# Performance work log

Measured on AMD Instinct MI355X. Metric: run time of the kernel, lower is better.

The kernel has to match this reference:

```python
import jax, jax.numpy as jnp
import numpy as np

D_MODEL = 128
NHEAD = 8
HEAD_DIM = D_MODEL // NHEAD  # 16
NUM_LAYERS = 7
NUM_LABELS = 2
N_NODES = 10000
N_EDGES = 160000
NEG_SLOPE = 0.2  # GATv2Conv default negative_slope


def setup_inputs() -> dict:
    key = jax.random.key(0)
    ks = jax.random.split(key, 10)
    s = 1.0 / np.sqrt(D_MODEL)
    inp = {}
    inp["x"] = jax.random.normal(ks[0], (N_NODES, D_MODEL), dtype=jnp.float32)
    inp["edge_index"] = jax.random.randint(ks[1], (2, N_EDGES), 0, N_NODES, dtype=jnp.int64)
    inp["nchunks"] = 8  # uniform extra chunk size -> chunk = NUM_LABELS + 8 = 10
    # per-layer GATv2 params, stacked on a leading layer axis
    inp["Wl"] = jax.random.normal(ks[2], (NUM_LAYERS, D_MODEL, NHEAD * HEAD_DIM), dtype=jnp.float32) * s
    inp["bl"] = jnp.zeros((NUM_LAYERS, NHEAD * HEAD_DIM), dtype=jnp.float32)
    inp["Wr"] = jax.random.normal(ks[3], (NUM_LAYERS, D_MODEL, NHEAD * HEAD_DIM), dtype=jnp.float32) * s
    inp["br"] = jnp.zeros((NUM_LAYERS, NHEAD * HEAD_DIM), dtype=jnp.float32)
    inp["att"] = jax.random.normal(ks[4], (NUM_LAYERS, NHEAD, HEAD_DIM), dtype=jnp.float32) * s
    inp["bias"] = jnp.zeros((NUM_LAYERS, NHEAD * HEAD_DIM), dtype=jnp.float32)
    # split head: Linear(d_model, 1)
    inp["w_head"] = jax.random.normal(ks[5], (D_MODEL, 1), dtype=jnp.float32) * s
    inp["b_head"] = jnp.zeros((1,), dtype=jnp.float32)
    return inp


def _gatv2_layer(x, src, dst, Wl, bl, Wr, br, att, bias):
    # GATv2: e_ij = a^T LeakyReLU(W_l x_j + W_r x_i); alpha = segment-softmax over dst; out_i = sum alpha * W_l x_j
    N = x.shape[0]
    xl = (x @ Wl + bl).reshape(N, NHEAD, HEAD_DIM)
    xr = (x @ Wr + br).reshape(N, NHEAD, HEAD_DIM)
    z = jax.nn.leaky_relu(xl[src] + xr[dst], NEG_SLOPE)          # [E, H, D]
    e = jnp.einsum('ehd,hd->eh', z, att)                          # [E, H]
    emax = jax.ops.segment_max(e, dst, num_segments=N)            # [N, H]
    ex = jnp.exp(e - emax[dst])
    denom = jax.ops.segment_sum(ex, dst, num_segments=N)          # [N, H]
    alpha = ex / (denom[dst] + 1e-16)                             # [E, H]
    out = jax.ops.segment_sum(alpha[..., None] * xl[src], dst, num_segments=N)  # [N, H, D]
    return out.reshape(N, NHEAD * HEAD_DIM) + bias


def reference(x, edge_index, nchunks, Wl, bl, Wr, br, att, bias, w_head, b_head):
    N = x.shape[0]
    loop = jnp.arange(N, dtype=edge_index.dtype)  # GATv2Conv add_self_loops=True
    src = jnp.concatenate([edge_index[0], loop])
    dst = jnp.concatenate([edge_index[1], loop])
    for i in range(NUM_LAYERS):
        x = _gatv2_layer(x, src, dst, Wl[i], bl[i], Wr[i], br[i], att[i], bias[i])
    # uniform split of size (NUM_LABELS + nchunks); keep first NUM_LABELS rows of each chunk
    chunk = NUM_LABELS + int(nchunks)
    xs = x.reshape(-1, chunk, D_MODEL)[:, :NUM_LABELS]            # [n_chunks, num_labels, d]
    out = (xs @ w_head + b_head)[..., 0]                          # [n_chunks, num_labels]
    return out
```

## Files before the change

### kernel.cpp

```cpp
#include <hip/hip_runtime.h>
#include <math.h>

typedef __attribute__((ext_vector_type(8))) short bf16x8;
typedef __attribute__((ext_vector_type(4))) float f32x4;

#define WFRAG (16 * 4 * 64 * 8)


__device__ inline int detect_is64(const int* __restrict__ ei) {
    int is64 = 1;
#pragma unroll
    for (int k = 1; k < 16; k += 2) is64 &= (ei[k] == 0);
    return is64;
}

__device__ inline void split1(float f, short& hi, short& lo) {
    unsigned u = __float_as_uint(f);
    hi = (short)(u >> 16);
    float fl = f - __uint_as_float(u & 0xffff0000u);
    lo = (short)(__float_as_uint(fl) >> 16);
}

__device__ inline void cvt8(const float4& a, const float4& b, bf16x8& hi, bf16x8& lo) {
    float f[8] = {a.x, a.y, a.z, a.w, b.x, b.y, b.z, b.w};
#pragma unroll
    for (int j = 0; j < 8; j++) {
        unsigned u = __float_as_uint(f[j]);
        hi[j] = (short)(u >> 16);
        float fl = f[j] - __uint_as_float(u & 0xffff0000u);
        lo[j] = (short)(__float_as_uint(fl) >> 16);
    }
}


__global__ __launch_bounds__(256) void prologue(const float* __restrict__ Wl,
                                                const float* __restrict__ Wr,
                                                short* __restrict__ Whi,
                                                short* __restrict__ Wlo,
                                                const float4* __restrict__ x4,
                                                short* __restrict__ cvH,
                                                short* __restrict__ cvL,
                                                const int* __restrict__ ei,
                                                int* __restrict__ deg,
                                                int N, int E) {
    __shared__ float Wt[128][17];
    int b = blockIdx.x, t = threadIdx.x;
    if (b < 112) {
        int l = b >> 4;
        int tile = b & 15;
        int c0 = tile * 16;
        const float* Wsrc = (c0 < 128) ? Wl + (size_t)l * 16384 : Wr + (size_t)l * 16384;
        int cbase = (c0 < 128) ? c0 : c0 - 128;
#pragma unroll
        for (int it = 0; it < 8; it++) {
            int idx = it * 256 + t;
            int k = idx >> 4, c = idx & 15;
            Wt[k][c] = Wsrc[(size_t)k * 128 + cbase + c];
        }
        __syncthreads();
        int kt = t >> 6, lane = t & 63, q = (lane >> 4), cl = lane & 15;
        bf16x8 hi, lo;
#pragma unroll
        for (int j = 0; j < 8; j++) {
            short h, lw;
            split1(Wt[kt * 32 + q * 8 + j][cl], h, lw);
            hi[j] = h; lo[j] = lw;
        }
        size_t off = ((((size_t)l * 16 + tile) * 4 + kt) * 64 + lane) * 8;
        *(bf16x8*)(Whi + off) = hi;
        *(bf16x8*)(Wlo + off) = lo;
        return;
    }
    int rb = b - 112;
    int RB = gridDim.x - 112;
    int n8 = N * 16;
    for (int id = rb * 256 + t; id < n8; id += RB * 256) {
        float4 a = x4[2 * id];
        float4 bb = x4[2 * id + 1];
        bf16x8 h, lw;
        cvt8(a, bb, h, lw);
        *(bf16x8*)(cvH + (size_t)id * 8) = h;
        *(bf16x8*)(cvL + (size_t)id * 8) = lw;
    }
    int is64 = detect_is64(ei);
    for (int e = rb * 256 + t; e < E; e += RB * 256) {
        long long pos = (long long)E + e;
        int d = ei[is64 ? 2 * pos : pos];
        if ((unsigned)d < (unsigned)N) atomicAdd(&deg[d], 1);
    }
}


__global__ __launch_bounds__(1024) void scan_kernel(const int* __restrict__ deg,
                                                    int* __restrict__ off,
                                                    int* __restrict__ cur, int N) {
    __shared__ int wsum[16];
    int t = threadIdx.x;
    int per = (N + 1023) >> 10;
    int b0 = t * per;
    int s = 0;
    for (int k = 0; k < per; k++) {
        int idx = b0 + k;
        if (idx < N) s += deg[idx];
    }
    int lane = t & 63, w = t >> 6;
    int v = s;
#pragma unroll
    for (int o = 1; o < 64; o <<= 1) {
        int u = __shfl_up(v, o, 64);
        if (lane >= o) v += u;
    }
    if (lane == 63) wsum[w] = v;
    __syncthreads();
    if (t == 0) {
        int r = 0;
#pragma unroll
        for (int j = 0; j < 16; j++) { int xx = wsum[j]; wsum[j] = r; r += xx; }
        off[N] = r;
    }
    __syncthreads();
    int run = v - s + wsum[w];
    for (int k = 0; k < per; k++) {
        int idx = b0 + k;
        if (idx < N) {
            off[idx] = run;
            cur[idx] = run;
            run += deg[idx];
        }
    }
}

__global__ void fill_kernel(const int* __restrict__ ei, int E, int N,
                            int* __restrict__ cur, int* __restrict__ esrc) {
    int e = blockIdx.x * blockDim.x + threadIdx.x;
    if (e >= E) return;
    int is64 = detect_is64(ei);
    long long spos = e, dpos = (long long)E + e;
    int s = ei[is64 ? 2 * spos : spos];
    int d = ei[is64 ? 2 * dpos : dpos];
    if ((unsigned)d >= (unsigned)N || (unsigned)s >= (unsigned)N) return;
    int p = atomicAdd(&cur[d], 1);
    esrc[p] = s;
}


__global__ __launch_bounds__(512, 1) void gemm_xlxr(const short* __restrict__ xhi,
                                                    const short* __restrict__ xlo,
                                                    const short* __restrict__ WhiL,
                                                    const short* __restrict__ WloL,
                                                    const float* __restrict__ blv,
                                                    const float* __restrict__ brv,
                                                    float* __restrict__ xl,
                                                    float* __restrict__ xr,
                                                    int N, int ntiles) {
    int t = threadIdx.x;
    int w = t >> 6, lane = t & 63, q = lane >> 4, cl = lane & 15;

    bf16x8 Bh[2][4], Bl[2][4];
    float biasv[2];
    float* op[2];
    int colc[2];
#pragma unroll
    for (int nt = 0; nt < 2; nt++) {
        int tile = w * 2 + nt;
        int col = tile * 16 + cl;
        if (col < 128) { biasv[nt] = blv[col]; op[nt] = xl; colc[nt] = col; }
        else           { biasv[nt] = brv[col - 128]; op[nt] = xr; colc[nt] = col - 128; }
#pragma unroll
        for (int kt = 0; kt < 4; kt++) {
            size_t o = (((size_t)tile * 4 + kt) * 64 + lane) * 8;
            Bh[nt][kt] = *(const bf16x8*)(WhiL + o);
            Bl[nt][kt] = *(const bf16x8*)(WloL + o);
        }
    }

    for (int rt = blockIdx.x; rt < ntiles; rt += gridDim.x) {
        int row = rt * 16 + cl;
        if (row >= N) row = N - 1;
        const short* ph = xhi + (size_t)row * 128 + q * 8;
        const short* pl = xlo + (size_t)row * 128 + q * 8;
        bf16x8 AH[4], AL[4];
#pragma unroll
        for (int kt = 0; kt < 4; kt++) {
            AH[kt] = *(const bf16x8*)(ph + kt * 32);
            AL[kt] = *(const bf16x8*)(pl + kt * 32);
        }

        f32x4 acc0 = {0.f, 0.f, 0.f, 0.f}, acc1 = {0.f, 0.f, 0.f, 0.f};
#pragma unroll
        for (int kt = 0; kt < 4; kt++) {
            acc0 = __builtin_amdgcn_mfma_f32_16x16x32_bf16(AH[kt], Bh[0][kt], acc0, 0, 0, 0);
            acc1 = __builtin_amdgcn_mfma_f32_16x16x32_bf16(AH[kt], Bh[1][kt], acc1, 0, 0, 0);
            acc0 = __builtin_amdgcn_mfma_f32_16x16x32_bf16(AL[kt], Bh[0][kt], acc0, 0, 0, 0);
            acc1 = __builtin_amdgcn_mfma_f32_16x16x32_bf16(AL[kt], Bh[1][kt], acc1, 0, 0, 0);
            acc0 = __builtin_amdgcn_mfma_f32_16x16x32_bf16(AH[kt], Bl[0][kt], acc0, 0, 0, 0);
            acc1 = __builtin_amdgcn_mfma_f32_16x16x32_bf16(AH[kt], Bl[1][kt], acc1, 0, 0, 0);
        }

#pragma unroll
        for (int nt = 0; nt < 2; nt++) {
            f32x4 a = nt ? acc1 : acc0;
#pragma unroll
            for (int r = 0; r < 4; r++) {
                int orow = rt * 16 + q * 4 + r;
                if (orow < N) op[nt][(size_t)orow * 128 + colc[nt]] = a[r] + biasv[nt];
            }
        }
    }
}


__device__ inline void agg_node(int i, int sub, int cl,
                                const float4* __restrict__ xl4, const float4* __restrict__ xr4,
                                const int* __restrict__ off, const int* __restrict__ esrc,
                                float4 atA, float4 atB, float4 bA, float4 bB,
                                float4& oA, float4& oB) {
    float4 xrA = xr4[(size_t)i * 32 + 2 * cl];
    float4 xrB = xr4[(size_t)i * 32 + 2 * cl + 1];
    int start = off[i];
    int total = off[i + 1] - start + 1;
    int groups = (total + 3) >> 2;

    int k0 = sub;
    int s0 = (k0 < total) ? ((k0 == 0) ? i : esrc[start + k0 - 1]) : i;
    int k1 = 4 + sub;
    int s1 = (k1 < total) ? esrc[start + k1 - 1] : i;
    float4 v0A = xl4[(size_t)s0 * 32 + 2 * cl];
    float4 v0B = xl4[(size_t)s0 * 32 + 2 * cl + 1];
    int k2 = 8 + sub;
    int s2 = (k2 < total) ? esrc[start + k2 - 1] : i;
    float4 v1A = xl4[(size_t)s1 * 32 + 2 * cl];
    float4 v1B = xl4[(size_t)s1 * 32 + 2 * cl + 1];

    float s = 0.f;
    float4 aA = make_float4(0.f, 0.f, 0.f, 0.f);
    float4 aB = make_float4(0.f, 0.f, 0.f, 0.f);

    for (int g = 0; g < groups; g++) {
        int k3 = 4 * (g + 3) + sub;
        int s3 = (k3 < total) ? esrc[start + k3 - 1] : i;
        float4 v2A = xl4[(size_t)s2 * 32 + 2 * cl];
        float4 v2B = xl4[(size_t)s2 * 32 + 2 * cl + 1];

        int kc = 4 * g + sub;
        int valid = kc < total;
        float z0 = v0A.x + xrA.x, z1 = v0A.y + xrA.y, z2 = v0A.z + xrA.z, z3 = v0A.w + xrA.w;
        float z4 = v0B.x + xrB.x, z5 = v0B.y + xrB.y, z6 = v0B.z + xrB.z, z7 = v0B.w + xrB.w;
        z0 = (z0 > 0.f) ? z0 : 0.2f * z0;
        z1 = (z1 > 0.f) ? z1 : 0.2f * z1;
        z2 = (z2 > 0.f) ? z2 : 0.2f * z2;
        z3 = (z3 > 0.f) ? z3 : 0.2f * z3;
        z4 = (z4 > 0.f) ? z4 : 0.2f * z4;
        z5 = (z5 > 0.f) ? z5 : 0.2f * z5;
        z6 = (z6 > 0.f) ? z6 : 0.2f * z6;
        z7 = (z7 > 0.f) ? z7 : 0.2f * z7;
        float p = z0 * atA.x + z1 * atA.y + z2 * atA.z + z3 * atA.w
                + z4 * atB.x + z5 * atB.y + z6 * atB.z + z7 * atB.w;
        p += __shfl_xor(p, 1, 64);
        p = fminf(fmaxf(p, -80.f), 80.f);
        float wgt = valid ? __expf(p) : 0.f;
        s += wgt;
        aA.x += wgt * v0A.x; aA.y += wgt * v0A.y; aA.z += wgt * v0A.z; aA.w += wgt * v0A.w;
        aB.x += wgt * v0B.x; aB.y += wgt * v0B.y; aB.z += wgt * v0B.z; aB.w += wgt * v0B.w;

        v0A = v1A; v0B = v1B;
        v1A = v2A; v1B = v2B;
        s2 = s3;
    }

#pragma unroll
    for (int o = 16; o <= 32; o <<= 1) {
        s += __shfl_xor(s, o, 64);
        aA.x += __shfl_xor(aA.x, o, 64); aA.y += __shfl_xor(aA.y, o, 64);
        aA.z += __shfl_xor(aA.z, o, 64); aA.w += __shfl_xor(aA.w, o, 64);
        aB.x += __shfl_xor(aB.x, o, 64); aB.y += __shfl_xor(aB.y, o, 64);
        aB.z += __shfl_xor(aB.z, o, 64); aB.w += __shfl_xor(aB.w, o, 64);
    }
    float inv = 1.f / (s + 1e-16f);
    oA.x = aA.x * inv + bA.x; oA.y = aA.y * inv + bA.y;
    oA.z = aA.z * inv + bA.z; oA.w = aA.w * inv + bA.w;
    oB.x = aB.x * inv + bB.x; oB.y = aB.y * inv + bB.y;
    oB.z = aB.z * inv + bB.z; oB.w = aB.w * inv + bB.w;
}


__global__ __launch_bounds__(256) void agg_gemm(const float4* __restrict__ xl4,
                                                const float4* __restrict__ xr4,
                                                const int* __restrict__ off,
                                                const int* __restrict__ esrc,
                                                const float4* __restrict__ att4,
                                                const float4* __restrict__ bias4,
                                                const short* __restrict__ WhiL,
                                                const short* __restrict__ WloL,
                                                const float* __restrict__ blv,
                                                const float* __restrict__ brv,
                                                float* __restrict__ xlo_out,
                                                float* __restrict__ xro_out,
                                                int N) {
    __shared__ __align__(16) short hiL[16 * 136];
    __shared__ __align__(16) short loL[16 * 136];
    int t = threadIdx.x;
    int w = t >> 6, lane = t & 63, sub = lane >> 4, cl = lane & 15, q = lane >> 4;
    int base = blockIdx.x * 16;

    float4 atA = att4[2 * cl];
    float4 atB = att4[2 * cl + 1];
    float4 bA = bias4[2 * cl], bB = bias4[2 * cl + 1];

    for (int j = 0; j < 4; j++) {
        int i = base + w * 4 + j;
        if (i < N) {
            float4 oA, oB;
            agg_node(i, sub, cl, xl4, xr4, off, esrc, atA, atB, bA, bB, oA, oB);
            if (sub == 0) {
                bf16x8 h, lw;
                cvt8(oA, oB, h, lw);
                int r = w * 4 + j;
                *(bf16x8*)&hiL[r * 136 + cl * 8] = h;
                *(bf16x8*)&loL[r * 136 + cl * 8] = lw;
            }
        }
    }
    __syncthreads();

    bf16x8 Ah[4], Al[4];
#pragma unroll
    for (int kt = 0; kt < 4; kt++) {
        Ah[kt] = *(const bf16x8*)&hiL[cl * 136 + kt * 32 + q * 8];
        Al[kt] = *(const bf16x8*)&loL[cl * 136 + kt * 32 + q * 8];
    }

#pragma unroll
    for (int tt = 0; tt < 4; tt++) {
        int tile = w * 4 + tt;
        int col = tile * 16 + cl;
        f32x4 acc = {0.f, 0.f, 0.f, 0.f};
#pragma unroll
        for (int kt = 0; kt < 4; kt++) {
            size_t o = (((size_t)tile * 4 + kt) * 64 + lane) * 8;
            bf16x8 bh = *(const bf16x8*)(WhiL + o);
            bf16x8 bl2 = *(const bf16x8*)(WloL + o);
            acc = __builtin_amdgcn_mfma_f32_16x16x32_bf16(Ah[kt], bh, acc, 0, 0, 0);
            acc = __builtin_amdgcn_mfma_f32_16x16x32_bf16(Al[kt], bh, acc, 0, 0, 0);
            acc = __builtin_amdgcn_mfma_f32_16x16x32_bf16(Ah[kt], bl2, acc, 0, 0, 0);
        }
        float biasv;
        float* op;
        int cc;
        if (col < 128) { biasv = blv[col]; op = xlo_out; cc = col; }
        else           { biasv = brv[col - 128]; op = xro_out; cc = col - 128; }
#pragma unroll
        for (int r = 0; r < 4; r++) {
            int row = base + q * 4 + r;
            if (row < N) op[(size_t)row * 128 + cc] = acc[r] + biasv;
        }
    }
}


__global__ __launch_bounds__(256) void gat_agg(const float4* __restrict__ xl4,
                                               const float4* __restrict__ xr4,
                                               const int* __restrict__ off,
                                               const int* __restrict__ esrc,
                                               const float4* __restrict__ att4,
                                               const float4* __restrict__ bias4,
                                               float4* __restrict__ out4, int N) {
    int lane = threadIdx.x & 63;
    int sub = lane >> 4;
    int cl = lane & 15;
    int i = blockIdx.x * 4 + (threadIdx.x >> 6);
    if (i >= N) return;
    float4 atA = att4[2 * cl];
    float4 atB = att4[2 * cl + 1];
    float4 bA = bias4[2 * cl], bB = bias4[2 * cl + 1];
    float4 oA, oB;
    agg_node(i, sub, cl, xl4, xr4, off, esrc, atA, atB, bA, bB, oA, oB);
    if (sub == 0) {
        out4[(size_t)i * 32 + 2 * cl] = oA;
        out4[(size_t)i * 32 + 2 * cl + 1] = oB;
    }
}


__global__ __launch_bounds__(128) void head_kernel(const float* __restrict__ x,
                                                   const float* __restrict__ w,
                                                   const float* __restrict__ bh,
                                                   const int* __restrict__ nch,
                                                   float* __restrict__ out) {
    __shared__ float r[2];
    int b = blockIdx.x, t = threadIdx.x;
    int chunk = 2 + nch[0];
    int row = (b >> 1) * chunk + (b & 1);
    float p = x[(size_t)row * 128 + t] * w[t];
#pragma unroll
    for (int o = 32; o >= 1; o >>= 1) p += __shfl_xor(p, o, 64);
    if ((t & 63) == 0) r[t >> 6] = p;
    __syncthreads();
    if (t == 0) out[b] = r[0] + r[1] + bh[0];
}


extern "C" void kernel_launch(void* const* d_in, const int* in_sizes, int n_in,
                              void* d_out, int out_size, void* d_ws, size_t ws_size,
                              hipStream_t stream) {
    const float* x0 = (const float*)d_in[0];
    const int* ei = (const int*)d_in[1];
    const int* nchunks = (const int*)d_in[2];
    const float* Wl = (const float*)d_in[3];
    const float* bl = (const float*)d_in[4];
    const float* Wr = (const float*)d_in[5];
    const float* br = (const float*)d_in[6];
    const float* att = (const float*)d_in[7];
    const float* bias = (const float*)d_in[8];
    const float* wh = (const float*)d_in[9];
    const float* bh = (const float*)d_in[10];

    const int D = 128;
    int N = in_sizes[0] / D;
    int E = in_sizes[1] / 2;
    int ntiles = (N + 15) / 16;

    size_t fN = (size_t)N * D;
    float* xlA = (float*)d_ws;
    float* xrA = xlA + fN;
    float* xlB = xrA + fN;
    float* xrB = xlB + fN;
    float* xout = xrB + fN;
    short* cvH0 = (short*)(xout + fN);
    short* cvL0 = cvH0 + fN;
    short* Whi = cvL0 + fN;
    short* Wlo = Whi + 7 * (size_t)WFRAG;
    int* deg = (int*)(Wlo + 7 * (size_t)WFRAG);
    int* off = deg + N;
    int* cur = off + N + 1;
    int* esrc = cur + N;

    hipMemsetAsync(deg, 0, (size_t)N * sizeof(int), stream);
    prologue<<<112 + 640, 256, 0, stream>>>(Wl, Wr, Whi, Wlo, (const float4*)x0,
                                            cvH0, cvL0, ei, deg, N, E);
    scan_kernel<<<1, 1024, 0, stream>>>(deg, off, cur, N);
    fill_kernel<<<(E + 255) / 256, 256, 0, stream>>>(ei, E, N, cur, esrc);

    gemm_xlxr<<<256, 512, 0, stream>>>(cvH0, cvL0, Whi, Wlo, bl, br, xlA, xrA, N, ntiles);

    for (int l = 0; l < 6; l++) {
        const float* rxl = (l % 2 == 0) ? xlA : xlB;
        const float* rxr = (l % 2 == 0) ? xrA : xrB;
        float* wxl = (l % 2 == 0) ? xlB : xlA;
        float* wxr = (l % 2 == 0) ? xrB : xrA;
        agg_gemm<<<ntiles, 256, 0, stream>>>((const float4*)rxl, (const float4*)rxr, off, esrc,
                                             (const float4*)(att + (size_t)l * D),
                                             (const float4*)(bias + (size_t)l * D),
                                             Whi + (size_t)(l + 1) * WFRAG,
                                             Wlo + (size_t)(l + 1) * WFRAG,
                                             bl + (size_t)(l + 1) * D,
                                             br + (size_t)(l + 1) * D,
                                             wxl, wxr, N);
    }

    gat_agg<<<(N + 3) / 4, 256, 0, stream>>>((const float4*)xlA, (const float4*)xrA, off, esrc,
                                             (const float4*)(att + 6 * (size_t)D),
                                             (const float4*)(bias + 6 * (size_t)D),
                                             (float4*)xout, N);

    head_kernel<<<out_size, 128, 0, stream>>>(xout, wh, bh, nchunks, (float*)d_out);
}
```

Measured before the change: 272.8 us.

## Fuse scan with first GEMM, enlarge agg_gemm tiles, fold head into final aggregation

Result: no change. 273.8 us (+0.4%).

```diff
diff --git a/kernel.cpp b/kernel.cpp
--- a/kernel.cpp
+++ b/kernel.cpp
@@ -91,41 +91,107 @@
 }
 
 
-__global__ __launch_bounds__(1024) void scan_kernel(const int* __restrict__ deg,
-                                                    int* __restrict__ off,
-                                                    int* __restrict__ cur, int N) {
-    __shared__ int wsum[16];
+__global__ __launch_bounds__(512, 1) void scan_gemm0(const int* __restrict__ deg,
+                                                     int* __restrict__ offp,
+                                                     int* __restrict__ cur, int N,
+                                                     const short* __restrict__ xhi,
+                                                     const short* __restrict__ xlo,
+                                                     const short* __restrict__ WhiL,
+                                                     const short* __restrict__ WloL,
+                                                     const float* __restrict__ blv,
+                                                     const float* __restrict__ brv,
+                                                     float* __restrict__ xl,
+                                                     float* __restrict__ xr,
+                                                     int ntiles) {
+    __shared__ int wsum[8];
     int t = threadIdx.x;
-    int per = (N + 1023) >> 10;
-    int b0 = t * per;
-    int s = 0;
-    for (int k = 0; k < per; k++) {
-        int idx = b0 + k;
-        if (idx < N) s += deg[idx];
-    }
-    int lane = t & 63, w = t >> 6;
-    int v = s;
-#pragma unroll
-    for (int o = 1; o < 64; o <<= 1) {
-        int u = __shfl_up(v, o, 64);
-        if (lane >= o) v += u;
-    }
-    if (lane == 63) wsum[w] = v;
-    __syncthreads();
-    if (t == 0) {
-        int r = 0;
-#pragma unroll
-        for (int j = 0; j < 16; j++) { int xx = wsum[j]; wsum[j] = r; r += xx; }
-        off[N] = r;
-    }
-    __syncthreads();
-    int run = v - s + wsum[w];
-    for (int k = 0; k < per; k++) {
-        int idx = b0 + k;
-        if (idx < N) {
-            off[idx] = run;
-            cur[idx] = run;
-            run += deg[idx];
+    if (blockIdx.x == 0) {
+        int per = (N + 511) >> 9;
+        int b0 = t * per;
+        int s = 0;
+        for (int k = 0; k < per; k++) {
+            int idx = b0 + k;
+            if (idx < N) s += deg[idx];
+        }
+        int lane = t & 63, w = t >> 6;
+        int v = s;
+#pragma unroll
+        for (int o = 1; o < 64; o <<= 1) {
+            int u = __shfl_up(v, o, 64);
+            if (lane >= o) v += u;
+        }
+        if (lane == 63) wsum[w] = v;
+        __syncthreads();
+        if (t == 0) {
+            int r = 0;
+#pragma unroll
+            for (int j = 0; j < 8; j++) { int xx = wsum[j]; wsum[j] = r; r += xx; }
+            offp[N] = r;
+        }
+        __syncthreads();
+        int run = v - s + wsum[w];
+        for (int k = 0; k < per; k++) {
+            int idx = b0 + k;
+            if (idx < N) {
+                offp[idx] = run;
+                cur[idx] = run;
+                run += deg[idx];
+            }
+        }
+        return;
+    }
+
+    int w = t >> 6, lane = t & 63, q = lane >> 4, cl = lane & 15;
+
+    bf16x8 Bh[2][4], Bl[2][4];
+    float biasv[2];
+    float* op[2];
+    int colc[2];
+#pragma unroll
+    for (int nt = 0; nt < 2; nt++) {
+        int tile = w * 2 + nt;
+        int col = tile * 16 + cl;
+        if (col < 128) { biasv[nt] = blv[col]; op[nt] = xl; colc[nt] = col; }
+        else           { biasv[nt] = brv[col - 128]; op[nt] = xr; colc[nt] = col - 128; }
+#pragma unroll
+        for (int kt = 0; kt < 4; kt++) {
+            size_t o = (((size_t)tile * 4 + kt) * 64 + lane) * 8;
+            Bh[nt][kt] = *(const bf16x8*)(WhiL + o);
+            Bl[nt][kt] = *(const bf16x8*)(WloL + o);
+        }
+    }
+
+    for (int rt = blockIdx.x - 1; rt < ntiles; rt += gridDim.x - 1) {
+        int row = rt * 16 + cl;
+        if (row >= N) row = N - 1;
+        const short* ph = xhi + (size_t)row * 128 + q * 8;
+        const short* pl = xlo + (size_t)row * 128 + q * 8;
+        bf16x8 AH[4], AL[4];
+#pragma unroll
+        for (int kt = 0; kt < 4; kt++) {
+            AH[kt] = *(const bf16x8*)(ph + kt * 32);
+            AL[kt] = *(const bf16x8*)(pl + kt * 32);
+        }
+
+        f32x4 acc0 = {0.f, 0.f, 0.f, 0.f}, acc1 = {0.f, 0.f, 0.f, 0.f};
+#pragma unroll
+        for (int kt = 0; kt < 4; kt++) {
+            acc0 = __builtin_amdgcn_mfma_f32_16x16x32_bf16(AH[kt], Bh[0][kt], acc0, 0, 0, 0);
+            acc1 = __builtin_amdgcn_mfma_f32_16x16x32_bf16(AH[kt], Bh[1][kt], acc1, 0, 0, 0);
+            acc0 = __builtin_amdgcn_mfma_f32_16x16x32_bf16(AL[kt], Bh[0][kt], acc0, 0, 0, 0);
+            acc1 = __builtin_amdgcn_mfma_f32_16x16x32_bf16(AL[kt], Bh[1][kt], acc1, 0, 0, 0);
+            acc0 = __builtin_amdgcn_mfma_f32_16x16x32_bf16(AH[kt], Bl[0][kt], acc0, 0, 0, 0);
+            acc1 = __builtin_amdgcn_mfma_f32_16x16x32_bf16(AH[kt], Bl[1][kt], acc1, 0, 0, 0);
+        }
+
+#pragma unroll
+        for (int nt = 0; nt < 2; nt++) {
+            f32x4 a = nt ? acc1 : acc0;
+#pragma unroll
+            for (int r = 0; r < 4; r++) {
+                int orow = rt * 16 + q * 4 + r;
+                if (orow < N) op[nt][(size_t)orow * 128 + colc[nt]] = a[r] + biasv[nt];
+            }
         }
     }
 }
@@ -141,72 +207,6 @@
     if ((unsigned)d >= (unsigned)N || (unsigned)s >= (unsigned)N) return;
     int p = atomicAdd(&cur[d], 1);
     esrc[p] = s;
-}
-
-
-__global__ __launch_bounds__(512, 1) void gemm_xlxr(const short* __restrict__ xhi,
-                                                    const short* __restrict__ xlo,
-                                                    const short* __restrict__ WhiL,
-                                                    const short* __restrict__ WloL,
-                                                    const float* __restrict__ blv,
-                                                    const float* __restrict__ brv,
-                                                    float* __restrict__ xl,
-                                                    float* __restrict__ xr,
-                                                    int N, int ntiles) {
-    int t = threadIdx.x;
-    int w = t >> 6, lane = t & 63, q = lane >> 4, cl = lane & 15;
-
-    bf16x8 Bh[2][4], Bl[2][4];
-    float biasv[2];
-    float* op[2];
-    int colc[2];
-#pragma unroll
-    for (int nt = 0; nt < 2; nt++) {
-        int tile = w * 2 + nt;
-        int col = tile * 16 + cl;
-        if (col < 128) { biasv[nt] = blv[col]; op[nt] = xl; colc[nt] = col; }
-        else           { biasv[nt] = brv[col - 128]; op[nt] = xr; colc[nt] = col - 128; }
-#pragma unroll
-        for (int kt = 0; kt < 4; kt++) {
-            size_t o = (((size_t)tile * 4 + kt) * 64 + lane) * 8;
-            Bh[nt][kt] = *(const bf16x8*)(WhiL + o);
-            Bl[nt][kt] = *(const bf16x8*)(WloL + o);
-        }
-    }
-
-    for (int rt = blockIdx.x; rt < ntiles; rt += gridDim.x) {
-        int row = rt * 16 + cl;
-        if (row >= N) row = N - 1;
-        const short* ph = xhi + (size_t)row * 128 + q * 8;
-        const short* pl = xlo + (size_t)row * 128 + q * 8;
-        bf16x8 AH[4], AL[4];
-#pragma unroll
-        for (int kt = 0; kt < 4; kt++) {
-            AH[kt] = *(const bf16x8*)(ph + kt * 32);
-            AL[kt] = *(const bf16x8*)(pl + kt * 32);
-        }
-
-        f32x4 acc0 = {0.f, 0.f, 0.f, 0.f}, acc1 = {0.f, 0.f, 0.f, 0.f};
-#pragma unroll
-        for (int kt = 0; kt < 4; kt++) {
-            acc0 = __builtin_amdgcn_mfma_f32_16x16x32_bf16(AH[kt], Bh[0][kt], acc0, 0, 0, 0);
-            acc1 = __builtin_amdgcn_mfma_f32_16x16x32_bf16(AH[kt], Bh[1][kt], acc1, 0, 0, 0);
-            acc0 = __builtin_amdgcn_mfma_f32_16x16x32_bf16(AL[kt], Bh[0][kt], acc0, 0, 0, 0);
-            acc1 = __builtin_amdgcn_mfma_f32_16x16x32_bf16(AL[kt], Bh[1][kt], acc1, 0, 0, 0);
-            acc0 = __builtin_amdgcn_mfma_f32_16x16x32_bf16(AH[kt], Bl[0][kt], acc0, 0, 0, 0);
-            acc1 = __builtin_amdgcn_mfma_f32_16x16x32_bf16(AH[kt], Bl[1][kt], acc1, 0, 0, 0);
-        }
-
-#pragma unroll
-        for (int nt = 0; nt < 2; nt++) {
-            f32x4 a = nt ? acc1 : acc0;
-#pragma unroll
-            for (int r = 0; r < 4; r++) {
-                int orow = rt * 16 + q * 4 + r;
-                if (orow < N) op[nt][(size_t)orow * 128 + colc[nt]] = a[r] + biasv[nt];
-            }
-        }
-    }
 }
 
 
@@ -284,24 +284,24 @@
 }
 
 
-__global__ __launch_bounds__(256) void agg_gemm(const float4* __restrict__ xl4,
-                                                const float4* __restrict__ xr4,
-                                                const int* __restrict__ off,
-                                                const int* __restrict__ esrc,
-                                                const float4* __restrict__ att4,
-                                                const float4* __restrict__ bias4,
-                                                const short* __restrict__ WhiL,
-                                                const short* __restrict__ WloL,
-                                                const float* __restrict__ blv,
-                                                const float* __restrict__ brv,
-                                                float* __restrict__ xlo_out,
-                                                float* __restrict__ xro_out,
-                                                int N) {
-    __shared__ __align__(16) short hiL[16 * 136];
-    __shared__ __align__(16) short loL[16 * 136];
+__global__ __launch_bounds__(512, 1) void agg_gemm(const float4* __restrict__ xl4,
+                                                   const float4* __restrict__ xr4,
+                                                   const int* __restrict__ off,
+                                                   const int* __restrict__ esrc,
+                                                   const float4* __restrict__ att4,
+                                                   const float4* __restrict__ bias4,
+                                                   const short* __restrict__ WhiL,
+                                                   const short* __restrict__ WloL,
+                                                   const float* __restrict__ blv,
+                                                   const float* __restrict__ brv,
+                                                   float* __restrict__ xlo_out,
+                                                   float* __restrict__ xro_out,
+                                                   int N) {
+    __shared__ __align__(16) short hiL[32 * 136];
+    __shared__ __align__(16) short loL[32 * 136];
     int t = threadIdx.x;
     int w = t >> 6, lane = t & 63, sub = lane >> 4, cl = lane & 15, q = lane >> 4;
-    int base = blockIdx.x * 16;
+    int base = blockIdx.x * 32;
 
     float4 atA = att4[2 * cl];
     float4 atB = att4[2 * cl + 1];
@@ -323,48 +323,62 @@
     }
     __syncthreads();
 
-    bf16x8 Ah[4], Al[4];
-#pragma unroll
-    for (int kt = 0; kt < 4; kt++) {
-        Ah[kt] = *(const bf16x8*)&hiL[cl * 136 + kt * 32 + q * 8];
-        Al[kt] = *(const bf16x8*)&loL[cl * 136 + kt * 32 + q * 8];
-    }
-
-#pragma unroll
-    for (int tt = 0; tt < 4; tt++) {
-        int tile = w * 4 + tt;
+    bf16x8 Bh[2][4], Bl[2][4];
+    float biasv[2];
+    float* op[2];
+    int cc[2];
+#pragma unroll
+    for (int tt = 0; tt < 2; tt++) {
+        int tile = w * 2 + tt;
         int col = tile * 16 + cl;
-        f32x4 acc = {0.f, 0.f, 0.f, 0.f};
+        if (col < 128) { biasv[tt] = blv[col]; op[tt] = xlo_out; cc[tt] = col; }
+        else           { biasv[tt] = brv[col - 128]; op[tt] = xro_out; cc[tt] = col - 128; }
 #pragma unroll
         for (int kt = 0; kt < 4; kt++) {
             size_t o = (((size_t)tile * 4 + kt) * 64 + lane) * 8;
-            bf16x8 bh = *(const bf16x8*)(WhiL + o);
-            bf16x8 bl2 = *(const bf16x8*)(WloL + o);
-            acc = __builtin_amdgcn_mfma_f32_16x16x32_bf16(Ah[kt], bh, acc, 0, 0, 0);
-            acc = __builtin_amdgcn_mfma_f32_16x16x32_bf16(Al[kt], bh, acc, 0, 0, 0);
-            acc = __builtin_amdgcn_mfma_f32_16x16x32_bf16(Ah[kt], bl2, acc, 0, 0, 0);
-        }
-        float biasv;
-        float* op;
-        int cc;
-        if (col < 128) { biasv = blv[col]; op = xlo_out; cc = col; }
-        else           { biasv = brv[col - 128]; op = xro_out; cc = col - 128; }
-#pragma unroll
-        for (int r = 0; r < 4; r++) {
-            int row = base + q * 4 + r;
-            if (row < N) op[(size_t)row * 128 + cc] = acc[r] + biasv;
-        }
-    }
-}
-
-
-__global__ __launch_bounds__(256) void gat_agg(const float4* __restrict__ xl4,
-                                               const float4* __restrict__ xr4,
-                                               const int* __restrict__ off,
-                                               const int* __restrict__ esrc,
-                                               const float4* __restrict__ att4,
-                                               const float4* __restrict__ bias4,
-                                               float4* __restrict__ out4, int N) {
+            Bh[tt][kt] = *(const bf16x8*)(WhiL + o);
+            Bl[tt][kt] = *(const bf16x8*)(WloL + o);
+        }
+    }
+
+#pragma unroll
+    for (int m = 0; m < 2; m++) {
+        bf16x8 Ah[4], Al[4];
+#pragma unroll
+        for (int kt = 0; kt < 4; kt++) {
+            Ah[kt] = *(const bf16x8*)&hiL[(m * 16 + cl) * 136 + kt * 32 + q * 8];
+            Al[kt] = *(const bf16x8*)&loL[(m * 16 + cl) * 136 + kt * 32 + q * 8];
+        }
+#pragma unroll
+        for (int tt = 0; tt < 2; tt++) {
+            f32x4 acc = {0.f, 0.f, 0.f, 0.f};
+#pragma unroll
+            for (int kt = 0; kt < 4; kt++) {
+                acc = __builtin_amdgcn_mfma_f32_16x16x32_bf16(Ah[kt], Bh[tt][kt], acc, 0, 0, 0);
+                acc = __builtin_amdgcn_mfma_f32_16x16x32_bf16(Al[kt], Bh[tt][kt], acc, 0, 0, 0);
+                acc = __builtin_amdgcn_mfma_f32_16x16x32_bf16(Ah[kt], Bl[tt][kt], acc, 0, 0, 0);
+            }
+#pragma unroll
+            for (int r = 0; r < 4; r++) {
+                int row = base + m * 16 + q * 4 + r;
+                if (row < N) op[tt][(size_t)row * 128 + cc[tt]] = acc[r] + biasv[tt];
+            }
+        }
+    }
+}
+
+
+__global__ __launch_bounds__(256) void gat_agg_head(const float4* __restrict__ xl4,
+                                                    const float4* __restrict__ xr4,
+                                                    const int* __restrict__ off,
+                                                    const int* __restrict__ esrc,
+                                                    const float4* __restrict__ att4,
+                                                    const float4* __restrict__ bias4,
+                                                    const float4* __restrict__ wh4,
+                                                    const float* __restrict__ bh,
+                                                    const int* __restrict__ nch,
+                                                    float* __restrict__ out,
+                                                    int n_out, int N) {
     int lane = threadIdx.x & 63;
     int sub = lane >> 4;
     int cl = lane & 15;
@@ -376,27 +390,20 @@
     float4 oA, oB;
     agg_node(i, sub, cl, xl4, xr4, off, esrc, atA, atB, bA, bB, oA, oB);
     if (sub == 0) {
-        out4[(size_t)i * 32 + 2 * cl] = oA;
-        out4[(size_t)i * 32 + 2 * cl + 1] = oB;
-    }
-}
-
-
-__global__ __launch_bounds__(128) void head_kernel(const float* __restrict__ x,
-                                                   const float* __restrict__ w,
-                                                   const float* __restrict__ bh,
-                                                   const int* __restrict__ nch,
-                                                   float* __restrict__ out) {
-    __shared__ float r[2];
-    int b = blockIdx.x, t = threadIdx.x;
-    int chunk = 2 + nch[0];
-    int row = (b >> 1) * chunk + (b & 1);
-    float p = x[(size_t)row * 128 + t] * w[t];
-#pragma unroll
-    for (int o = 32; o >= 1; o >>= 1) p += __shfl_xor(p, o, 64);
-    if ((t & 63) == 0) r[t >> 6] = p;
-    __syncthreads();
-    if (t == 0) out[b] = r[0] + r[1] + bh[0];
+        int chunk = 2 + nch[0];
+        int r = i % chunk;
+        if (r < 2) {
+            float4 wa = wh4[2 * cl], wb = wh4[2 * cl + 1];
+            float p = oA.x * wa.x + oA.y * wa.y + oA.z * wa.z + oA.w * wa.w
+                    + oB.x * wb.x + oB.y * wb.y + oB.z * wb.z + oB.w * wb.w;
+#pragma unroll
+            for (int o = 1; o <= 8; o <<= 1) p += __shfl_xor(p, o, 64);
+            if (cl == 0) {
+                int b = (i / chunk) * 2 + r;
+                if (b < n_out) out[b] = p + bh[0];
+            }
+        }
+    }
 }
 
 
@@ -425,8 +432,7 @@
     float* xrA = xlA + fN;
     float* xlB = xrA + fN;
     float* xrB = xlB + fN;
-    float* xout = xrB + fN;
-    short* cvH0 = (short*)(xout + fN);
+    short* cvH0 = (short*)(xrB + fN);
     short* cvL0 = cvH0 + fN;
     short* Whi = cvL0 + fN;
     short* Wlo = Whi + 7 * (size_t)WFRAG;
@@ -438,30 +444,30 @@
     hipMemsetAsync(deg, 0, (size_t)N * sizeof(int), stream);
     prologue<<<112 + 640, 256, 0, stream>>>(Wl, Wr, Whi, Wlo, (const float4*)x0,
                                             cvH0, cvL0, ei, deg, N, E);
-    scan_kernel<<<1, 1024, 0, stream>>>(deg, off, cur, N);
+    scan_gemm0<<<257, 512, 0, stream>>>(deg, off, cur, N, cvH0, cvL0, Whi, Wlo,
+                                        bl, br, xlA, xrA, ntiles);
     fill_kernel<<<(E + 255) / 256, 256, 0, stream>>>(ei, E, N, cur, esrc);
 
-    gemm_xlxr<<<256, 512, 0, stream>>>(cvH0, cvL0, Whi, Wlo, bl, br, xlA, xrA, N, ntiles);
-
+    int ablocks = (N + 31) / 32;
     for (int l = 0; l < 6; l++) {
         const float* rxl = (l % 2 == 0) ? xlA : xlB;
         const float* rxr = (l % 2 == 0) ? xrA : xrB;
         float* wxl = (l % 2 == 0) ? xlB : xlA;
         float* wxr = (l % 2 == 0) ? xrB : xrA;
-        agg_gemm<<<ntiles, 256, 0, stream>>>((const float4*)rxl, (const float4*)rxr, off, esrc,
-                                             (const float4*)(att + (size_t)l * D),
-                                             (const float4*)(bias + (size_t)l * D),
-                                             Whi + (size_t)(l + 1) * WFRAG,
-                                             Wlo + (size_t)(l + 1) * WFRAG,
-                                             bl + (size_t)(l + 1) * D,
-                                             br + (size_t)(l + 1) * D,
-                                             wxl, wxr, N);
-    }
-
-    gat_agg<<<(N + 3) / 4, 256, 0, stream>>>((const float4*)xlA, (const float4*)xrA, off, esrc,
-                                             (const float4*)(att + 6 * (size_t)D),
-                                             (const float4*)(bias + 6 * (size_t)D),
-                                             (float4*)xout, N);
-
-    head_kernel<<<out_size, 128, 0, stream>>>(xout, wh, bh, nchunks, (float*)d_out);
-}
+        agg_gemm<<<ablocks, 512, 0, stream>>>((const float4*)rxl, (const float4*)rxr, off, esrc,
+                                              (const float4*)(att + (size_t)l * D),
+                                              (const float4*)(bias + (size_t)l * D),
+                                              Whi + (size_t)(l + 1) * WFRAG,
+                                              Wlo + (size_t)(l + 1) * WFRAG,
+                                              bl + (size_t)(l + 1) * D,
+                                              br + (size_t)(l + 1) * D,
+                                              wxl, wxr, N);
+    }
+
+    gat_agg_head<<<(N + 3) / 4, 256, 0, stream>>>((const float4*)xlA, (const float4*)xrA,
+                                                  off, esrc,
+                                                  (const float4*)(att + 6 * (size_t)D),
+                                                  (const float4*)(bias + 6 * (size_t)D),
+                                                  (const float4*)wh, bh, nchunks,
+                                                  (float*)d_out, out_size, N);
+}
```
